# Optimization experiments

Measured on AMD Instinct MI355X. Metric: run time of the kernel, lower is better.

## Reference

```python
import jax, jax.numpy as jnp
import numpy as np

B, Q, K, D = 32, 1024, 1024, 128

def setup_inputs() -> dict:
    key = jax.random.key(0)
    kq, kk, kv, kl = jax.random.split(key, 4)
    return {
        "queries": jax.random.normal(kq, (B, Q, D), dtype=jnp.float32),
        "keys": jax.random.normal(kk, (B, K, D), dtype=jnp.float32),
        "values": jax.random.normal(kv, (B, K, D), dtype=jnp.float32),
        "valid_length": jax.random.randint(kl, (B,), 1, K + 1),
    }

def reference(queries, keys, values, valid_length):
    d = queries.shape[-1]
    # scores: [B, Q, K]
    scores = jnp.einsum("bqd,bkd->bqk", queries, keys) / jnp.sqrt(jnp.float32(d))
    # length mask: position k is valid iff k < valid_length[b]
    mask = jnp.arange(keys.shape[1])[None, None, :] < valid_length[:, None, None]
    scores = jnp.where(mask, scores, jnp.float32(-1e9))
    attn = jax.nn.softmax(scores, axis=-1)
    # dropout module is identity in eval / p=0
    return jnp.einsum("bqk,bkv->bqv", attn, values)
```

## Files before the change

kernel.cpp:

```cpp
#include <hip/hip_runtime.h>
#include <hip/hip_bf16.h>
#include <stdint.h>

#define B_    32
#define QLEN  1024
#define KSEQ  1024
#define DIM   128
#define NKT   (KSEQ / 64)
#define SCALE 0.08838834764831845f

typedef __attribute__((ext_vector_type(8)))  short short8;
typedef __attribute__((ext_vector_type(4)))  float floatx4;
typedef __attribute__((ext_vector_type(16))) float floatx16;
typedef unsigned int u32;

__device__ __forceinline__ u32 f2bf(float x) {
  union { float f; u32 u; } v; v.f = x;
  return (v.u + 0x7FFF + ((v.u >> 16) & 1)) >> 16;
}
__device__ __forceinline__ u32 pack2(float lo, float hi) {
  return f2bf(lo) | (f2bf(hi) << 16);
}
__device__ __forceinline__ u32 cvtpk(float lo, float hi) {
  u32 d;
  asm("v_cvt_pk_bf16_f32 %0, %1, %2" : "=v"(d) : "v"(lo), "v"(hi));
  return d;
}
__device__ __forceinline__ void swap32(u32& a, u32& b) {
  asm volatile("v_permlane32_swap_b32 %0, %1" : "+v"(a), "+v"(b));
}
typedef union { uint4 u; short8 s; } U8;

__device__ __forceinline__ void barrier_full() {
  asm volatile("s_waitcnt vmcnt(0) lgkmcnt(0)" ::: "memory");
  __syncthreads();
}

__global__ __launch_bounds__(256) void prep_kernel(const float* __restrict__ Kg,
                                                   const float* __restrict__ Vg,
                                                   const int* __restrict__ vlen,
                                                   uint4* __restrict__ Ksw,
                                                   uint4* __restrict__ Vsw,
                                                   int2* __restrict__ task) {
  __shared__ __align__(16) u32 Vu[64 * 65];
  __shared__ int sidx[32];
  const int kt = blockIdx.x, b = blockIdx.y, t = threadIdx.x;
  const bool tableblk = (blockIdx.z == 0) && (kt == 0) && (b == 0);

  if (tableblk && t < 64) {
    const int bb = t & 31;
    const int ntb = (vlen[bb] + 63) >> 6;
    int rank = 0;
#pragma unroll
    for (int j = 0; j < 32; j++) {
      const int ntj = __shfl(ntb, j);
      rank += (ntj > ntb) | ((ntj == ntb) & (j < bb));
    }
    if (t < 32) sidx[rank] = bb;
  }

  if (kt * 64 < vlen[b]) {
    if (blockIdx.z == 0) {
      const float* src = Kg + ((size_t)b * KSEQ + kt * 64) * DIM;
      uint4* dst = Ksw + ((size_t)b * NKT + kt) * 1024;
#pragma unroll
      for (int it = 0; it < 4; it++) {
        const int f = it * 256 + t, r = f >> 4, c = f & 15;
        floatx4 f0 = *(const floatx4*)(src + r * DIM + c * 8);
        floatx4 f1 = *(const floatx4*)(src + r * DIM + c * 8 + 4);
        uint4 o;
        o.x = pack2(f0[0], f0[1]); o.y = pack2(f0[2], f0[3]);
        o.z = pack2(f1[0], f1[1]); o.w = pack2(f1[2], f1[3]);
        dst[r * 16 + (c ^ (r & 15))] = o;
      }
    } else {
      const float* src = Vg + ((size_t)b * KSEQ + kt * 64) * DIM;
#pragma unroll
      for (int it = 0; it < 8; it++) {
        const int k = it * 8 + (t >> 5), c = t & 31;
        const floatx4 f = *(const floatx4*)(src + (size_t)k * DIM + c * 4);
        const int s = (k >> 3) & 4;
        Vu[k * 65 + ((2 * c) ^ s)]     = pack2(f[0], f[1]);
        Vu[k * 65 + ((2 * c + 1) ^ s)] = pack2(f[2], f[3]);
      }
      __syncthreads();
      uint4* dst = Vsw + ((size_t)b * NKT + kt) * 1024;
#pragma unroll
      for (int it = 0; it < 4; it++) {
        const int id = it * 256 + t;
        const int kc = id & 7, d = (id >> 3) & 127;
        const int col = (d >> 1) ^ (kc & 4);
        u32 r[8];
#pragma unroll
        for (int j = 0; j < 8; j++) r[j] = Vu[(kc * 8 + j) * 65 + col];
        const u32 sel = (d & 1) ? 0x07060302u : 0x05040100u;
        uint4 o;
        o.x = __builtin_amdgcn_perm(r[1], r[0], sel);
        o.y = __builtin_amdgcn_perm(r[3], r[2], sel);
        o.z = __builtin_amdgcn_perm(r[5], r[4], sel);
        o.w = __builtin_amdgcn_perm(r[7], r[6], sel);
        dst[d * 8 + (kc ^ (d & 7))] = o;
      }
    }
  }

  if (tableblk) {
    __syncthreads();
    for (int l = t; l < 512; l += 256) {
      const int x = l & 7, j = l >> 3;
      int rank, q;
      if (j < 32) { rank = (j & 1) ? x + 8  : x;      q = j >> 1; }
      else        { rank = (j & 1) ? x + 16 : x + 24; q = (j - 32) >> 1; }
      task[l] = make_int2(sidx[rank], q << 6);
    }
  }
}

typedef const __attribute__((address_space(1))) u32* as1p;
typedef __attribute__((address_space(3))) u32* as3p;
__device__ __forceinline__ void gl_lds16(const void* g, void* l) {
  __builtin_amdgcn_global_load_lds((as1p)g, (as3p)l, 16, 0, 0);
}

__global__ __launch_bounds__(128, 1) void attn_kernel(
    const float* __restrict__ Qg, const uint4* __restrict__ Ksw,
    const uint4* __restrict__ Vsw, const int* __restrict__ vlen,
    const int2* __restrict__ task, float* __restrict__ Og) {
  __shared__ __align__(16) short Kbuf[2][64 * 128];
  __shared__ __align__(16) short Vbuf[2][128 * 64];

  const int2 tq = task[blockIdx.x];
  const int b = tq.x, q0 = tq.y;
  const int t = threadIdx.x, wave = t >> 6, lane = t & 63;
  const int l31 = lane & 31, hi = lane >> 5, m15 = l31 & 15, m7 = l31 & 7;
  const int L  = vlen[b];
  const int nt = (L + 63) >> 6;

  const char* Kt = (const char*)(Ksw + (size_t)b * NKT * 1024);
  const char* Vt = (const char*)(Vsw + (size_t)b * NKT * 1024);

  short8 qb[8];
  {
    const float* qrow = Qg + ((size_t)b * QLEN + q0 + wave * 32 + l31) * DIM;
#pragma unroll
    for (int c = 0; c < 8; c++) {
      floatx4 f0 = *(const floatx4*)(qrow + c * 16 + hi * 8);
      floatx4 f1 = *(const floatx4*)(qrow + c * 16 + hi * 8 + 4);
      short8 a;
      a[0] = (short)f2bf(f0[0]); a[1] = (short)f2bf(f0[1]);
      a[2] = (short)f2bf(f0[2]); a[3] = (short)f2bf(f0[3]);
      a[4] = (short)f2bf(f1[0]); a[5] = (short)f2bf(f1[1]);
      a[6] = (short)f2bf(f1[2]); a[7] = (short)f2bf(f1[3]);
      qb[c] = a;
    }
  }

  float lrow = 0.0f;
  floatx16 oacc[4];
#pragma unroll
  for (int dt = 0; dt < 4; dt++)
#pragma unroll
    for (int i = 0; i < 16; i++) oacc[dt][i] = 0.0f;

#define ISSUE_K(tk, bb)                                                        \
  {                                                                            \
    const char* g_ = Kt + (size_t)(tk) * 16384 + wave * 8192 + lane * 16;      \
    _Pragma("unroll") for (int i_ = 0; i_ < 8; i_++)                           \
        gl_lds16(g_ + i_ * 1024, (char*)Kbuf[bb] + wave * 8192 + i_ * 1024);   \
  }
#define ISSUE_V(tk, bb)                                                        \
  {                                                                            \
    const char* g_ = Vt + (size_t)(tk) * 16384 + wave * 8192 + lane * 16;      \
    _Pragma("unroll") for (int i_ = 0; i_ < 8; i_++)                           \
        gl_lds16(g_ + i_ * 1024, (char*)Vbuf[bb] + wave * 8192 + i_ * 1024);   \
  }

  ISSUE_K(0, 0);
  ISSUE_V(0, 0);

#define PV_TILE(SV, KC0, KC1)                                                  \
  {                                                                            \
    u32 u0 = cvtpk(SV[0], SV[1]),   u1 = cvtpk(SV[2], SV[3]);                  \
    u32 u2 = cvtpk(SV[4], SV[5]),   u3 = cvtpk(SV[6], SV[7]);                  \
    swap32(u0, u2); swap32(u1, u3);                                            \
    u32 w0 = cvtpk(SV[8], SV[9]),   w1 = cvtpk(SV[10], SV[11]);                \
    u32 w2 = cvtpk(SV[12], SV[13]), w3 = cvtpk(SV[14], SV[15]);                \
    swap32(w0, w2); swap32(w1, w3);                                            \
    U8 pu0; pu0.u.x = u0; pu0.u.y = u1; pu0.u.z = u2; pu0.u.w = u3;            \
    U8 pu1; pu1.u.x = w0; pu1.u.y = w1; pu1.u.z = w2; pu1.u.w = w3;            \
    __builtin_amdgcn_s_setprio(1);                                             \
    _Pragma("unroll") for (int dt = 0; dt < 4; dt++) {                         \
      const short* vr_ = Vb_ + (dt * 32 + l31) * 64;                           \
      const short8 b0_ = *(const short8*)(vr_ + ((KC0) ^ m7) * 8);             \
      oacc[dt] = __builtin_amdgcn_mfma_f32_32x32x16_bf16(pu0.s, b0_, oacc[dt], 0, 0, 0); \
      const short8 b1_ = *(const short8*)(vr_ + ((KC1) ^ m7) * 8);             \
      oacc[dt] = __builtin_amdgcn_mfma_f32_32x32x16_bf16(pu1.s, b1_, oacc[dt], 0, 0, 0); \
    }                                                                          \
    __builtin_amdgcn_s_setprio(0);                                             \
  }

  for (int tk = 0; tk < nt; tk++) {
    const int k0 = tk * 64;
    barrier_full();
    if (tk + 1 < nt) {
      ISSUE_K(tk + 1, (tk + 1) & 1);
      ISSUE_V(tk + 1, (tk + 1) & 1);
    }
    const short* Kb_ = Kbuf[tk & 1];
    const short* Vb_ = Vbuf[tk & 1];

    floatx16 s0, s1;
#pragma unroll
    for (int i = 0; i < 16; i++) { s0[i] = 0.0f; s1[i] = 0.0f; }
    {
      const short* kr0 = Kb_ + l31 * 128;
      const short* kr1 = Kb_ + (32 + l31) * 128;
      __builtin_amdgcn_s_setprio(1);
#pragma unroll
      for (int c = 0; c < 8; c++) {
        const int cp = ((2 * c + hi) ^ m15) * 8;
        const short8 ka0 = *(const short8*)(kr0 + cp);
        const short8 ka1 = *(const short8*)(kr1 + cp);
        s0 = __builtin_amdgcn_mfma_f32_32x32x16_bf16(ka0, qb[c], s0, 0, 0, 0);
        s1 = __builtin_amdgcn_mfma_f32_32x32x16_bf16(ka1, qb[c], s1, 0, 0, 0);
      }
      __builtin_amdgcn_s_setprio(0);
    }

    if (k0 + 64 <= L) {
#pragma unroll
      for (int r = 0; r < 16; r++) {
        s0[r] = __expf(fminf(s0[r] * SCALE, 30.0f));
        s1[r] = __expf(fminf(s1[r] * SCALE, 30.0f));
        lrow += s0[r] + s1[r];
      }
    } else {
#pragma unroll
      for (int r = 0; r < 16; r++) {
        const int ck = (r & 3) + 8 * (r >> 2) + 4 * hi;
        const float a0 = (k0 + ck < L)      ? __expf(fminf(s0[r] * SCALE, 30.0f)) : 0.0f;
        const float a1 = (k0 + 32 + ck < L) ? __expf(fminf(s1[r] * SCALE, 30.0f)) : 0.0f;
        s0[r] = a0; s1[r] = a1;
        lrow += a0 + a1;
      }
    }

    PV_TILE(s0, 0 + hi, 2 + hi);
    PV_TILE(s1, 4 + hi, 6 + hi);
  }

  lrow += __shfl_xor(lrow, 32);
  const float inv_ = 1.0f / lrow;
  float iv[16];
#pragma unroll
  for (int r = 0; r < 16; r++)
    iv[r] = __shfl(inv_, (r & 3) + 8 * (r >> 2) + 4 * hi);
  float* obase = Og + ((size_t)b * QLEN + q0 + wave * 32) * DIM + l31;
#pragma unroll
  for (int dt = 0; dt < 4; dt++) {
#pragma unroll
    for (int r = 0; r < 16; r++) {
      const int rq = (r & 3) + 8 * (r >> 2) + 4 * hi;
      obase[(size_t)rq * DIM + dt * 32] = oacc[dt][r] * iv[r];
    }
  }
#undef ISSUE_K
#undef ISSUE_V
#undef PV_TILE
}

extern "C" void kernel_launch(void* const* d_in, const int* in_sizes, int n_in,
                              void* d_out, int out_size, void* d_ws, size_t ws_size,
                              hipStream_t stream) {
  const float* Qg = (const float*)d_in[0];
  const float* Kg = (const float*)d_in[1];
  const float* Vg = (const float*)d_in[2];
  const int*  vln = (const int*)d_in[3];
  uint4* Ksw = (uint4*)d_ws;
  uint4* Vsw = (uint4*)((char*)d_ws + (size_t)B_ * NKT * 16384);
  int2*  Tsk = (int2*)((char*)d_ws + 2 * (size_t)B_ * NKT * 16384);

  prep_kernel<<<dim3(NKT, B_, 2), 256, 0, stream>>>(Kg, Vg, vln, Ksw, Vsw, Tsk);
  attn_kernel<<<dim3(512), 128, 0, stream>>>(Qg, Ksw, Vsw, vln, Tsk,
                                             (float*)d_out);
}
```

Measured before the change: 124.4 us.

## Split key tile across two wave pairs and load V directly to registers

Doubles the block to four waves: each pair of waves handles the same 32 query rows but a different 32-key half of each 64-key tile. The two partial output accumulators and row sums are then combined through LDS at the end. V is no longer staged in LDS and is read from global memory straight into registers, which halves the LDS footprint. This is meant to raise per-CU parallelism and latency hiding, at the cost of a final cross-wave reduction and uncached global V loads on the critical path of each iteration.

Measured after the change: 116.8 us. 6.1% less time.

```diff
diff --git a/kernel.cpp b/kernel.cpp
--- a/kernel.cpp
+++ b/kernel.cpp
@@ -122,26 +122,27 @@
   __builtin_amdgcn_global_load_lds((as1p)g, (as3p)l, 16, 0, 0);
 }
 
-__global__ __launch_bounds__(128, 1) void attn_kernel(
+__global__ __launch_bounds__(256, 2) void attn_kernel(
     const float* __restrict__ Qg, const uint4* __restrict__ Ksw,
     const uint4* __restrict__ Vsw, const int* __restrict__ vlen,
     const int2* __restrict__ task, float* __restrict__ Og) {
   __shared__ __align__(16) short Kbuf[2][64 * 128];
-  __shared__ __align__(16) short Vbuf[2][128 * 64];
+  __shared__ float Lred[2][32];
 
   const int2 tq = task[blockIdx.x];
   const int b = tq.x, q0 = tq.y;
   const int t = threadIdx.x, wave = t >> 6, lane = t & 63;
+  const int qh = wave & 1, kh = wave >> 1;
   const int l31 = lane & 31, hi = lane >> 5, m15 = l31 & 15, m7 = l31 & 7;
   const int L  = vlen[b];
   const int nt = (L + 63) >> 6;
 
-  const char* Kt = (const char*)(Ksw + (size_t)b * NKT * 1024);
-  const char* Vt = (const char*)(Vsw + (size_t)b * NKT * 1024);
+  const char*  Kt = (const char*)(Ksw + (size_t)b * NKT * 1024);
+  const short* Vt = (const short*)(Vsw + (size_t)b * NKT * 1024);
 
   short8 qb[8];
   {
-    const float* qrow = Qg + ((size_t)b * QLEN + q0 + wave * 32 + l31) * DIM;
+    const float* qrow = Qg + ((size_t)b * QLEN + q0 + qh * 32 + l31) * DIM;
 #pragma unroll
     for (int c = 0; c < 8; c++) {
       floatx4 f0 = *(const floatx4*)(qrow + c * 16 + hi * 8);
@@ -164,109 +165,111 @@
 
 #define ISSUE_K(tk, bb)                                                        \
   {                                                                            \
-    const char* g_ = Kt + (size_t)(tk) * 16384 + wave * 8192 + lane * 16;      \
-    _Pragma("unroll") for (int i_ = 0; i_ < 8; i_++)                           \
-        gl_lds16(g_ + i_ * 1024, (char*)Kbuf[bb] + wave * 8192 + i_ * 1024);   \
-  }
-#define ISSUE_V(tk, bb)                                                        \
-  {                                                                            \
-    const char* g_ = Vt + (size_t)(tk) * 16384 + wave * 8192 + lane * 16;      \
-    _Pragma("unroll") for (int i_ = 0; i_ < 8; i_++)                           \
-        gl_lds16(g_ + i_ * 1024, (char*)Vbuf[bb] + wave * 8192 + i_ * 1024);   \
+    const char* g_ = Kt + (size_t)(tk) * 16384 + wave * 4096 + lane * 16;      \
+    _Pragma("unroll") for (int i_ = 0; i_ < 4; i_++)                           \
+        gl_lds16(g_ + i_ * 1024, (char*)Kbuf[bb] + wave * 4096 + i_ * 1024);   \
   }
 
   ISSUE_K(0, 0);
-  ISSUE_V(0, 0);
-
-#define PV_TILE(SV, KC0, KC1)                                                  \
-  {                                                                            \
-    u32 u0 = cvtpk(SV[0], SV[1]),   u1 = cvtpk(SV[2], SV[3]);                  \
-    u32 u2 = cvtpk(SV[4], SV[5]),   u3 = cvtpk(SV[6], SV[7]);                  \
-    swap32(u0, u2); swap32(u1, u3);                                            \
-    u32 w0 = cvtpk(SV[8], SV[9]),   w1 = cvtpk(SV[10], SV[11]);                \
-    u32 w2 = cvtpk(SV[12], SV[13]), w3 = cvtpk(SV[14], SV[15]);                \
-    swap32(w0, w2); swap32(w1, w3);                                            \
-    U8 pu0; pu0.u.x = u0; pu0.u.y = u1; pu0.u.z = u2; pu0.u.w = u3;            \
-    U8 pu1; pu1.u.x = w0; pu1.u.y = w1; pu1.u.z = w2; pu1.u.w = w3;            \
-    __builtin_amdgcn_s_setprio(1);                                             \
-    _Pragma("unroll") for (int dt = 0; dt < 4; dt++) {                         \
-      const short* vr_ = Vb_ + (dt * 32 + l31) * 64;                           \
-      const short8 b0_ = *(const short8*)(vr_ + ((KC0) ^ m7) * 8);             \
-      oacc[dt] = __builtin_amdgcn_mfma_f32_32x32x16_bf16(pu0.s, b0_, oacc[dt], 0, 0, 0); \
-      const short8 b1_ = *(const short8*)(vr_ + ((KC1) ^ m7) * 8);             \
-      oacc[dt] = __builtin_amdgcn_mfma_f32_32x32x16_bf16(pu1.s, b1_, oacc[dt], 0, 0, 0); \
-    }                                                                          \
-    __builtin_amdgcn_s_setprio(0);                                             \
-  }
 
   for (int tk = 0; tk < nt; tk++) {
     const int k0 = tk * 64;
     barrier_full();
-    if (tk + 1 < nt) {
-      ISSUE_K(tk + 1, (tk + 1) & 1);
-      ISSUE_V(tk + 1, (tk + 1) & 1);
-    }
+    if (tk + 1 < nt) ISSUE_K(tk + 1, (tk + 1) & 1);
     const short* Kb_ = Kbuf[tk & 1];
-    const short* Vb_ = Vbuf[tk & 1];
-
-    floatx16 s0, s1;
-#pragma unroll
-    for (int i = 0; i < 16; i++) { s0[i] = 0.0f; s1[i] = 0.0f; }
+
+    short8 vb[4][2];
     {
-      const short* kr0 = Kb_ + l31 * 128;
-      const short* kr1 = Kb_ + (32 + l31) * 128;
+      const short* vt_ = Vt + (size_t)tk * 8192;
+#pragma unroll
+      for (int dt = 0; dt < 4; dt++) {
+        const short* vr_ = vt_ + (dt * 32 + l31) * 64;
+        vb[dt][0] = *(const short8*)(vr_ + ((kh * 4 + 0 + hi) ^ m7) * 8);
+        vb[dt][1] = *(const short8*)(vr_ + ((kh * 4 + 2 + hi) ^ m7) * 8);
+      }
+    }
+
+    floatx16 s;
+#pragma unroll
+    for (int i = 0; i < 16; i++) s[i] = 0.0f;
+    {
+      const short* kr = Kb_ + (kh * 32 + l31) * 128;
       __builtin_amdgcn_s_setprio(1);
 #pragma unroll
       for (int c = 0; c < 8; c++) {
-        const int cp = ((2 * c + hi) ^ m15) * 8;
-        const short8 ka0 = *(const short8*)(kr0 + cp);
-        const short8 ka1 = *(const short8*)(kr1 + cp);
-        s0 = __builtin_amdgcn_mfma_f32_32x32x16_bf16(ka0, qb[c], s0, 0, 0, 0);
-        s1 = __builtin_amdgcn_mfma_f32_32x32x16_bf16(ka1, qb[c], s1, 0, 0, 0);
+        const short8 ka = *(const short8*)(kr + ((2 * c + hi) ^ m15) * 8);
+        s = __builtin_amdgcn_mfma_f32_32x32x16_bf16(ka, qb[c], s, 0, 0, 0);
       }
       __builtin_amdgcn_s_setprio(0);
     }
 
-    if (k0 + 64 <= L) {
+    if (k0 + kh * 32 + 32 <= L) {
 #pragma unroll
       for (int r = 0; r < 16; r++) {
-        s0[r] = __expf(fminf(s0[r] * SCALE, 30.0f));
-        s1[r] = __expf(fminf(s1[r] * SCALE, 30.0f));
-        lrow += s0[r] + s1[r];
+        s[r] = __expf(fminf(s[r] * SCALE, 30.0f));
+        lrow += s[r];
       }
     } else {
 #pragma unroll
       for (int r = 0; r < 16; r++) {
         const int ck = (r & 3) + 8 * (r >> 2) + 4 * hi;
-        const float a0 = (k0 + ck < L)      ? __expf(fminf(s0[r] * SCALE, 30.0f)) : 0.0f;
-        const float a1 = (k0 + 32 + ck < L) ? __expf(fminf(s1[r] * SCALE, 30.0f)) : 0.0f;
-        s0[r] = a0; s1[r] = a1;
-        lrow += a0 + a1;
-      }
-    }
-
-    PV_TILE(s0, 0 + hi, 2 + hi);
-    PV_TILE(s1, 4 + hi, 6 + hi);
+        const float a = (k0 + kh * 32 + ck < L)
+                            ? __expf(fminf(s[r] * SCALE, 30.0f)) : 0.0f;
+        s[r] = a;
+        lrow += a;
+      }
+    }
+
+    {
+      u32 u0 = cvtpk(s[0], s[1]),   u1 = cvtpk(s[2], s[3]);
+      u32 u2 = cvtpk(s[4], s[5]),   u3 = cvtpk(s[6], s[7]);
+      swap32(u0, u2); swap32(u1, u3);
+      u32 w0 = cvtpk(s[8], s[9]),   w1 = cvtpk(s[10], s[11]);
+      u32 w2 = cvtpk(s[12], s[13]), w3 = cvtpk(s[14], s[15]);
+      swap32(w0, w2); swap32(w1, w3);
+      U8 pu0; pu0.u.x = u0; pu0.u.y = u1; pu0.u.z = u2; pu0.u.w = u3;
+      U8 pu1; pu1.u.x = w0; pu1.u.y = w1; pu1.u.z = w2; pu1.u.w = w3;
+      __builtin_amdgcn_s_setprio(1);
+#pragma unroll
+      for (int dt = 0; dt < 4; dt++) {
+        oacc[dt] = __builtin_amdgcn_mfma_f32_32x32x16_bf16(pu0.s, vb[dt][0], oacc[dt], 0, 0, 0);
+        oacc[dt] = __builtin_amdgcn_mfma_f32_32x32x16_bf16(pu1.s, vb[dt][1], oacc[dt], 0, 0, 0);
+      }
+      __builtin_amdgcn_s_setprio(0);
+    }
   }
 
   lrow += __shfl_xor(lrow, 32);
-  const float inv_ = 1.0f / lrow;
-  float iv[16];
-#pragma unroll
-  for (int r = 0; r < 16; r++)
-    iv[r] = __shfl(inv_, (r & 3) + 8 * (r >> 2) + 4 * hi);
-  float* obase = Og + ((size_t)b * QLEN + q0 + wave * 32) * DIM + l31;
-#pragma unroll
-  for (int dt = 0; dt < 4; dt++) {
-#pragma unroll
-    for (int r = 0; r < 16; r++) {
-      const int rq = (r & 3) + 8 * (r >> 2) + 4 * hi;
-      obase[(size_t)rq * DIM + dt * 32] = oacc[dt][r] * iv[r];
+  barrier_full();
+  float* scr = (float*)Kbuf;
+  if (kh == 1) {
+    if (lane < 32) Lred[qh][l31] = lrow;
+#pragma unroll
+    for (int dt = 0; dt < 4; dt++)
+#pragma unroll
+      for (int r = 0; r < 16; r++)
+        scr[(dt * 16 + r) * 128 + qh * 64 + lane] = oacc[dt][r];
+  }
+  __syncthreads();
+  if (kh == 0) {
+    const float ltot = lrow + Lred[qh][l31];
+    const float inv_ = 1.0f / ltot;
+    float iv[16];
+#pragma unroll
+    for (int r = 0; r < 16; r++)
+      iv[r] = __shfl(inv_, (r & 3) + 8 * (r >> 2) + 4 * hi);
+    float* obase = Og + ((size_t)b * QLEN + q0 + qh * 32) * DIM + l31;
+#pragma unroll
+    for (int dt = 0; dt < 4; dt++) {
+#pragma unroll
+      for (int r = 0; r < 16; r++) {
+        const int rq = (r & 3) + 8 * (r >> 2) + 4 * hi;
+        const float v = oacc[dt][r] + scr[(dt * 16 + r) * 128 + qh * 64 + lane];
+        obase[(size_t)rq * DIM + dt * 32] = v * iv[r];
+      }
     }
   }
 #undef ISSUE_K
-#undef ISSUE_V
-#undef PV_TILE
 }
 
 extern "C" void kernel_launch(void* const* d_in, const int* in_sizes, int n_in,
@@ -281,6 +284,6 @@
   int2*  Tsk = (int2*)((char*)d_ws + 2 * (size_t)B_ * NKT * 16384);
 
   prep_kernel<<<dim3(NKT, B_, 2), 256, 0, stream>>>(Kg, Vg, vln, Ksw, Vsw, Tsk);
-  attn_kernel<<<dim3(512), 128, 0, stream>>>(Qg, Ksw, Vsw, vln, Tsk,
+  attn_kernel<<<dim3(512), 256, 0, stream>>>(Qg, Ksw, Vsw, vln, Tsk,
                                              (float*)d_out);
 }
```
